# Performance work log

Measured on AMD Instinct MI355X. Metric: run time of the kernel, lower is better.

The kernel has to match this reference:

```python
import jax, jax.numpy as jnp
import numpy as np

GRID_SIZE = 5
SPLINE_ORDER = 3
HIDDEN = 128
IN_FT = 768
BATCH = 32768

def make_grid():
    # uniform grid on [-1, 1] extended by spline_order knots on each side
    h = 2.0 / GRID_SIZE
    return (jnp.arange(-SPLINE_ORDER, GRID_SIZE + SPLINE_ORDER + 1, dtype=jnp.float32) * h - 1.0)

def b_splines(x, grid):
    # x: (B, in) -> bases: (B, in, GRID_SIZE + SPLINE_ORDER) via Cox-de-Boor recursion
    xe = x[..., None]                                  # (B, in, 1)
    bases = ((xe >= grid[:-1]) & (xe < grid[1:])).astype(x.dtype)
    for k in range(1, SPLINE_ORDER + 1):
        left = (xe - grid[:-(k + 1)]) / (grid[k:-1] - grid[:-(k + 1)]) * bases[..., :-1]
        right = (grid[k + 1:] - xe) / (grid[k + 1:] - grid[1:-k]) * bases[..., 1:]
        bases = left + right
    return bases

def kan_layer(x, base_w, spline_w, grid):
    # base_w: (out, in); spline_w: (out, in, G+k)
    B = x.shape[0]
    base_out = jax.nn.silu(x) @ base_w.T
    bas = b_splines(x, grid).reshape(B, -1)            # (B, in*(G+k))
    spline_out = bas @ spline_w.reshape(spline_w.shape[0], -1).T
    return base_out + spline_out

def setup_inputs() -> dict:
    key = jax.random.key(0)
    ks = jax.random.split(key, 8)
    nb = GRID_SIZE + SPLINE_ORDER  # 8 basis functions per edge
    return {
        "stm": jax.random.uniform(ks[0], (BATCH, IN_FT), dtype=jnp.float32),
        "nstm": jax.random.uniform(ks[1], (BATCH, IN_FT), dtype=jnp.float32),
        "ft_w": jax.random.normal(ks[2], (HIDDEN, IN_FT), dtype=jnp.float32) * 0.02,
        "ft_b": jnp.zeros((HIDDEN,), dtype=jnp.float32),
        "kan1_base_w": jax.random.normal(ks[3], (HIDDEN, 2 * HIDDEN), dtype=jnp.float32) * 0.05,
        "kan1_spline_w": jax.random.normal(ks[4], (HIDDEN, 2 * HIDDEN, nb), dtype=jnp.float32) * 0.05,
        "kan2_base_w": jax.random.normal(ks[5], (1, HIDDEN), dtype=jnp.float32) * 0.05,
        "kan2_spline_w": jax.random.normal(ks[6], (1, HIDDEN, nb), dtype=jnp.float32) * 0.05,
    }

def reference(stm, nstm, ft_w, ft_b, kan1_base_w, kan1_spline_w, kan2_base_w, kan2_spline_w):
    grid = make_grid()
    stm_h = stm @ ft_w.T + ft_b
    nstm_h = nstm @ ft_w.T + ft_b
    hidden = jnp.concatenate([stm_h, nstm_h], axis=1)   # (B, 2*HIDDEN)
    hidden = kan_layer(hidden, kan1_base_w, kan1_spline_w, grid)
    out = kan_layer(hidden, kan2_base_w, kan2_spline_w, grid)
    return jax.nn.sigmoid(out)
```

## Files before the change

### kernel.cpp

```cpp
#include <hip/hip_runtime.h>
#include <hip/hip_bf16.h>
#include <math.h>
#include <stdint.h>

typedef __attribute__((ext_vector_type(8))) short bf16x8;
typedef __attribute__((ext_vector_type(4))) float f32x4;

#define SH 260

__device__ __forceinline__ uint32_t pack2(float a, float b) {
    union { __hip_bfloat162 h2; uint32_t u; } c;
    c.h2 = __float22bfloat162_rn(make_float2(a, b));
    return c.u;
}
__device__ __forceinline__ unsigned short f2bf(float f) {
    union { __hip_bfloat16 h; unsigned short u; } c;
    c.h = __float2bfloat16(f);
    return c.u;
}
__device__ __forceinline__ float bf2f(unsigned short h) {
    union { uint32_t u; float f; } c; c.u = ((uint32_t)h) << 16;
    return c.f;
}
__device__ __forceinline__ float silu_f(float x) {
    return x / (1.0f + __expf(-x));
}

__device__ __forceinline__ void bspline8(float x, float* __restrict__ b) {
    const float tt = (x + 2.2f) * 2.5f;
#pragma unroll
    for (int v = 0; v < 8; ++v) {
        float y = fabsf(tt - (float)(v + 2));
        float p = fmaxf(2.0f - y, 0.0f);
        float q = fmaxf(1.0f - y, 0.0f);
        b[v] = (p * p * p - 4.0f * q * q * q) * (1.0f / 6.0f);
    }
}

__device__ __forceinline__ void gload16(const void* g, void* l) {
    __builtin_amdgcn_global_load_lds(
        (const __attribute__((address_space(1))) void*)g,
        (__attribute__((address_space(3))) void*)l, 16, 0, 0);
}

__global__ __launch_bounds__(256) void prep_ftw(const float* __restrict__ ftw,
                                                unsigned short* __restrict__ Wb) {
    const int idx = blockIdx.x * 256 + threadIdx.x;
    Wb[idx] = f2bf(ftw[idx]);
}

__global__ __launch_bounds__(256) void prep_bp(const float* __restrict__ bw,
                                               const float* __restrict__ sw,
                                               unsigned short* __restrict__ Bp) {
    const int idx = blockIdx.x * 256 + threadIdx.x;
    const int n = idx >> 12;
    const int k = idx & 4095;
    const int f = k >> 4;
    const int v = k & 15;
    float val = 0.f;
    if (v == 0) val = bw[n * 256 + f];
    else if (v <= 8) val = sw[(size_t)(n * 256 + f) * 8 + (v - 1)];
    Bp[idx] = f2bf(val);
}

__global__ __launch_bounds__(512) void kan_fused(
        const float* __restrict__ stm, const float* __restrict__ nstm,
        const unsigned short* __restrict__ Wb, const float* __restrict__ bias,
        const unsigned short* __restrict__ Bp,
        const float* __restrict__ w2b, const float* __restrict__ w2s,
        float* __restrict__ out) {
    __shared__ alignas(16) char lds[132096];
    char* smA = lds;
    char* smB = lds + 32768;
    unsigned short* smH = (unsigned short*)(lds + 65536);

    const int r0 = blockIdx.x * 128;
    const int t = threadIdx.x;
    const int l = t & 63, w = t >> 6;
    const int fr = l & 15, h = l >> 4;

    const int wrF = w >> 1, wcF = w & 1;
    const int arowb = w * 16 + (l >> 5);
    const int acol = (l & 31) * 4;

    float4 regY[8];
    f32x4 facc[2][4];
#pragma unroll
    for (int mt = 0; mt < 2; ++mt)
#pragma unroll
        for (int nt = 0; nt < 4; ++nt) facc[mt][nt] = (f32x4){0.f, 0.f, 0.f, 0.f};

#pragma unroll
    for (int q = 0; q < 8; ++q)
        regY[q] = *reinterpret_cast<const float4*>(
            &stm[(size_t)(r0 + arowb + q * 2) * 768 + acol]);

#pragma unroll 1
    for (int tk = 0; tk < 12; ++tk) {
        const int k0 = (tk >= 6 ? tk - 6 : tk) * 128;
#pragma unroll
        for (int q = 0; q < 8; ++q) {
            const int rowA = arowb + q * 2;
            int2 wv;
            wv.x = (int)pack2(regY[q].x, regY[q].y);
            wv.y = (int)pack2(regY[q].z, regY[q].w);
            const uint32_t dst = (uint32_t)rowA * 256u +
                ((uint32_t)((((l & 31) >> 1)) ^ (rowA & 15)) << 4) +
                (uint32_t)(l & 1) * 8u;
            *reinterpret_cast<int2*>(smA + dst) = wv;
        }
#pragma unroll
        for (int j = 0; j < 4; ++j) {
            const int idx = w * 4 + j;
            const int col = idx * 4 + (l >> 4);
            gload16(&Wb[(size_t)col * 768 + k0 + (((l & 15) ^ (col & 15)) << 3)],
                    smB + idx * 1024);
        }
        if (tk < 11) {
            const int nk = tk + 1;
            const float* __restrict__ Ap = (nk >= 6) ? nstm : stm;
            const int nk0 = (nk >= 6 ? nk - 6 : nk) * 128;
#pragma unroll
            for (int q = 0; q < 8; ++q)
                regY[q] = *reinterpret_cast<const float4*>(
                    &Ap[(size_t)(r0 + arowb + q * 2) * 768 + nk0 + acol]);
            asm volatile("s_waitcnt vmcnt(8)" ::: "memory");
        } else {
            asm volatile("s_waitcnt vmcnt(0)" ::: "memory");
        }
        asm volatile("s_waitcnt lgkmcnt(0)" ::: "memory");
        __builtin_amdgcn_sched_barrier(0);
        __builtin_amdgcn_s_barrier();
#pragma unroll
        for (int ks = 0; ks < 4; ++ks) {
            bf16x8 a[2], b[4];
#pragma unroll
            for (int mt = 0; mt < 2; ++mt) {
                const uint32_t row = (uint32_t)(wrF * 32 + mt * 16 + fr);
                a[mt] = *reinterpret_cast<const bf16x8*>(
                    smA + row * 256u +
                    (((uint32_t)(ks * 4 + h) ^ (row & 15u)) << 4));
            }
#pragma unroll
            for (int nt = 0; nt < 4; ++nt) {
                const uint32_t col = (uint32_t)(wcF * 64 + nt * 16 + fr);
                b[nt] = *reinterpret_cast<const bf16x8*>(
                    smB + col * 256u +
                    (((uint32_t)(ks * 4 + h) ^ (col & 15u)) << 4));
            }
#pragma unroll
            for (int mt = 0; mt < 2; ++mt)
#pragma unroll
                for (int nt = 0; nt < 4; ++nt)
                    facc[mt][nt] = __builtin_amdgcn_mfma_f32_16x16x32_bf16(
                        a[mt], b[nt], facc[mt][nt], 0, 0, 0);
        }
        if (tk == 5 || tk == 11) {
            const int so = (tk == 11) ? 128 : 0;
#pragma unroll
            for (int nt = 0; nt < 4; ++nt) {
                const int colL = wcF * 64 + nt * 16 + fr;
                const float bv = bias[colL];
#pragma unroll
                for (int mt = 0; mt < 2; ++mt) {
#pragma unroll
                    for (int j = 0; j < 4; ++j) {
                        const int row = wrF * 32 + mt * 16 + h * 4 + j;
                        smH[row * SH + so + colL] = f2bf(facc[mt][nt][j] + bv);
                    }
                    facc[mt][nt] = (f32x4){0.f, 0.f, 0.f, 0.f};
                }
            }
        }
        asm volatile("s_waitcnt lgkmcnt(0)" ::: "memory");
        __builtin_amdgcn_sched_barrier(0);
        __builtin_amdgcn_s_barrier();
    }

    const int wrK = w >> 2, wcK = w & 3;
    const int xrow = t & 127, xq = t >> 7;
    f32x4 kacc[4][2];
#pragma unroll
    for (int mt = 0; mt < 4; ++mt)
#pragma unroll
        for (int nt = 0; nt < 2; ++nt) kacc[mt][nt] = (f32x4){0.f, 0.f, 0.f, 0.f};

#pragma unroll 1
    for (int jb = 0; jb < 32; ++jb) {
#pragma unroll
        for (int j = 0; j < 4; ++j) {
            const int idx = w * 4 + j;
            const int col = idx * 4 + (l >> 4);
            gload16(&Bp[(size_t)col * 4096 + jb * 128 +
                        (((l & 15) ^ (col & 15)) << 3)],
                    smB + idx * 1024);
        }
        {
            const uint32_t xx = *reinterpret_cast<const uint32_t*>(
                reinterpret_cast<const char*>(smH) +
                ((size_t)xrow * SH + jb * 8 + xq * 2) * 2);
#pragma unroll
            for (int e = 0; e < 2; ++e) {
                const float x =
                    bf2f((unsigned short)(e ? (xx >> 16) : (xx & 0xffffu)));
                float bs[8];
                bspline8(x, bs);
                const uint32_t w0 = pack2(silu_f(x), bs[0]);
                const uint32_t w1 = pack2(bs[1], bs[2]);
                const uint32_t w2 = pack2(bs[3], bs[4]);
                const uint32_t w3 = pack2(bs[5], bs[6]);
                const uint32_t w4 = pack2(bs[7], 0.f);
                const int f = xq * 2 + e;
                const uint32_t base = (uint32_t)xrow * 256u;
                const uint32_t s0 = (uint32_t)((2 * f) ^ (xrow & 15)) << 4;
                const uint32_t s1 = (uint32_t)((2 * f + 1) ^ (xrow & 15)) << 4;
                *reinterpret_cast<int4*>(smA + base + s0) =
                    make_int4((int)w0, (int)w1, (int)w2, (int)w3);
                *reinterpret_cast<int4*>(smA + base + s1) =
                    make_int4((int)w4, 0, 0, 0);
            }
        }
        asm volatile("s_waitcnt vmcnt(0) lgkmcnt(0)" ::: "memory");
        __builtin_amdgcn_sched_barrier(0);
        __builtin_amdgcn_s_barrier();
#pragma unroll
        for (int ks = 0; ks < 4; ++ks) {
            bf16x8 a[4], b[2];
#pragma unroll
            for (int mt = 0; mt < 4; ++mt) {
                const uint32_t row = (uint32_t)(wrK * 64 + mt * 16 + fr);
                a[mt] = *reinterpret_cast<const bf16x8*>(
                    smA + row * 256u +
                    (((uint32_t)(ks * 4 + h) ^ (row & 15u)) << 4));
            }
#pragma unroll
            for (int nt = 0; nt < 2; ++nt) {
                const uint32_t col = (uint32_t)(wcK * 32 + nt * 16 + fr);
                b[nt] = *reinterpret_cast<const bf16x8*>(
                    smB + col * 256u +
                    (((uint32_t)(ks * 4 + h) ^ (col & 15u)) << 4));
            }
#pragma unroll
            for (int mt = 0; mt < 4; ++mt)
#pragma unroll
                for (int nt = 0; nt < 2; ++nt)
                    kacc[mt][nt] = __builtin_amdgcn_mfma_f32_16x16x32_bf16(
                        a[mt], b[nt], kacc[mt][nt], 0, 0, 0);
        }
        asm volatile("s_waitcnt lgkmcnt(0)" ::: "memory");
        __builtin_amdgcn_sched_barrier(0);
        __builtin_amdgcn_s_barrier();
    }

    unsigned short* smH2 = (unsigned short*)lds;
#pragma unroll
    for (int mt = 0; mt < 4; ++mt)
#pragma unroll
        for (int nt = 0; nt < 2; ++nt) {
            const int col = wcK * 32 + nt * 16 + fr;
#pragma unroll
            for (int j = 0; j < 4; ++j) {
                const int row = wrK * 64 + mt * 16 + h * 4 + j;
                smH2[row * 136 + col] = f2bf(kacc[mt][nt][j]);
            }
        }
    __syncthreads();
    const int row2 = t >> 2, qd = t & 3;
    float sum = 0.f;
#pragma unroll 4
    for (int i = 0; i < 32; ++i) {
        const int j = qd * 32 + ((i + qd * 8) & 31);
        const float x = bf2f(smH2[row2 * 136 + j]);
        float bs[8];
        bspline8(x, bs);
        const float4 s0 = *reinterpret_cast<const float4*>(&w2s[j * 8]);
        const float4 s1 = *reinterpret_cast<const float4*>(&w2s[j * 8 + 4]);
        float s = silu_f(x) * w2b[j];
        s += bs[0] * s0.x + bs[1] * s0.y + bs[2] * s0.z + bs[3] * s0.w;
        s += bs[4] * s1.x + bs[5] * s1.y + bs[6] * s1.z + bs[7] * s1.w;
        sum += s;
    }
    sum += __shfl_xor(sum, 1, 64);
    sum += __shfl_xor(sum, 2, 64);
    if (qd == 0) out[r0 + row2] = 1.0f / (1.0f + __expf(-sum));
}

extern "C" void kernel_launch(void* const* d_in, const int* in_sizes, int n_in,
                              void* d_out, int out_size, void* d_ws, size_t ws_size,
                              hipStream_t stream) {
    const float* stm  = (const float*)d_in[0];
    const float* nstm = (const float*)d_in[1];
    const float* ft_w = (const float*)d_in[2];
    const float* ft_b = (const float*)d_in[3];
    const float* k1bw = (const float*)d_in[4];
    const float* k1sw = (const float*)d_in[5];
    const float* k2bw = (const float*)d_in[6];
    const float* k2sw = (const float*)d_in[7];
    float* out = (float*)d_out;

    char* ws = (char*)d_ws;
    unsigned short* Wb = (unsigned short*)ws;
    unsigned short* Bp = (unsigned short*)(ws + 196608);

    prep_ftw<<<384, 256, 0, stream>>>(ft_w, Wb);
    prep_bp<<<2048, 256, 0, stream>>>(k1bw, k1sw, Bp);
    kan_fused<<<256, 512, 0, stream>>>(stm, nstm, Wb, ft_b, Bp, k2bw, k2sw, out);
}
```

Baseline: 115.6 us.

## Halve row tile to 64, double grid, transpose hidden layout, add setprio

The fused kernel now handles 64 rows per block instead of 128 and launches 512 blocks instead of 256. It stores the first-layer hidden activations transposed with a swizzle so each wave expands one feature across 64 rows during the spline stage. LDS use drops from about 129 KB to 80 KB so more blocks can be resident per CU, which should improve latency hiding and balance across the 256 CUs. The feature GEMM loop is unrolled by two with double-buffered register prefetch, and MFMA phases run at raised priority. The trade-off is that each Wb and Bp weight tile is reloaded twice as often, and each MFMA step does less work.

```diff
diff --git a/kernel.cpp b/kernel.cpp
--- a/kernel.cpp
+++ b/kernel.cpp
@@ -5,8 +5,6 @@
 
 typedef __attribute__((ext_vector_type(8))) short bf16x8;
 typedef __attribute__((ext_vector_type(4))) float f32x4;
-
-#define SH 260
 
 __device__ __forceinline__ uint32_t pack2(float a, float b) {
     union { __hip_bfloat162 h2; uint32_t u; } c;
@@ -63,213 +61,212 @@
     Bp[idx] = f2bf(val);
 }
 
-__global__ __launch_bounds__(512) void kan_fused(
+__global__ __launch_bounds__(512, 4) void kan_fused(
         const float* __restrict__ stm, const float* __restrict__ nstm,
         const unsigned short* __restrict__ Wb, const float* __restrict__ bias,
         const unsigned short* __restrict__ Bp,
         const float* __restrict__ w2b, const float* __restrict__ w2s,
         float* __restrict__ out) {
-    __shared__ alignas(16) char lds[132096];
-    char* smA = lds;
-    char* smB = lds + 32768;
-    unsigned short* smH = (unsigned short*)(lds + 65536);
-
-    const int r0 = blockIdx.x * 128;
+    __shared__ alignas(16) char lds[81920];
+    char* smA  = lds;
+    char* smB  = lds + 16384;
+    char* smHT = lds + 49152;
+
+    const int r0 = blockIdx.x * 64;
     const int t = threadIdx.x;
     const int l = t & 63, w = t >> 6;
     const int fr = l & 15, h = l >> 4;
-
-    const int wrF = w >> 1, wcF = w & 1;
-    const int arowb = w * 16 + (l >> 5);
-    const int acol = (l & 31) * 4;
-
-    float4 regY[8];
-    f32x4 facc[2][4];
+    const int wr = w >> 2, wc = w & 3;
+
+    const int arow = t >> 3;
+    const int acol = (t & 7) * 16;
+    const uint32_t adst0 = (uint32_t)arow * 256u +
+        ((uint32_t)(((t & 7) * 2) ^ (arow & 15)) << 4);
+    const uint32_t adst1 = (uint32_t)arow * 256u +
+        ((uint32_t)(((t & 7) * 2 + 1) ^ (arow & 15)) << 4);
+    const int gidx = w * 4;
+
+    f32x4 acc[2][2];
 #pragma unroll
     for (int mt = 0; mt < 2; ++mt)
 #pragma unroll
-        for (int nt = 0; nt < 4; ++nt) facc[mt][nt] = (f32x4){0.f, 0.f, 0.f, 0.f};
-
-#pragma unroll
-    for (int q = 0; q < 8; ++q)
-        regY[q] = *reinterpret_cast<const float4*>(
-            &stm[(size_t)(r0 + arowb + q * 2) * 768 + acol]);
-
+        for (int nt = 0; nt < 2; ++nt) acc[mt][nt] = (f32x4){0.f, 0.f, 0.f, 0.f};
+
+    float4 regY[4], regZ[4];
+
+#define FT_ISSUE(REG, TK)                                                      \
+    {                                                                          \
+        const float* __restrict__ Ap = ((TK) >= 6) ? nstm : stm;               \
+        const int kk = ((TK) % 6) * 128;                                       \
+        _Pragma("unroll") for (int q = 0; q < 4; ++q)                          \
+            REG[q] = *reinterpret_cast<const float4*>(                         \
+                &Ap[(size_t)(r0 + arow) * 768 + kk + acol + q * 4]);           \
+    }
+
+#define FT_WRITE(REG)                                                          \
+    {                                                                          \
+        int4 w0, w1;                                                           \
+        w0.x = (int)pack2(REG[0].x, REG[0].y);                                 \
+        w0.y = (int)pack2(REG[0].z, REG[0].w);                                 \
+        w0.z = (int)pack2(REG[1].x, REG[1].y);                                 \
+        w0.w = (int)pack2(REG[1].z, REG[1].w);                                 \
+        w1.x = (int)pack2(REG[2].x, REG[2].y);                                 \
+        w1.y = (int)pack2(REG[2].z, REG[2].w);                                 \
+        w1.z = (int)pack2(REG[3].x, REG[3].y);                                 \
+        w1.w = (int)pack2(REG[3].z, REG[3].w);                                 \
+        *reinterpret_cast<int4*>(smA + adst0) = w0;                            \
+        *reinterpret_cast<int4*>(smA + adst1) = w1;                            \
+    }
+
+#define GLOADB_FT(K0)                                                          \
+    _Pragma("unroll") for (int j = 0; j < 4; ++j) {                            \
+        const int col = (gidx + j) * 4 + (l >> 4);                             \
+        gload16(&Wb[(size_t)col * 768 + (K0) + (((l & 15) ^ (col & 15)) << 3)],\
+                smB + (gidx + j) * 1024);                                      \
+    }
+
+#define GEMM_STEP()                                                            \
+    _Pragma("unroll") for (int ks = 0; ks < 4; ++ks) {                         \
+        bf16x8 a[2], b[2];                                                     \
+        _Pragma("unroll") for (int mt = 0; mt < 2; ++mt) {                     \
+            const uint32_t row = (uint32_t)(wr * 32 + mt * 16 + fr);           \
+            a[mt] = *reinterpret_cast<const bf16x8*>(                          \
+                smA + row * 256u +                                             \
+                (((uint32_t)(ks * 4 + h) ^ (row & 15u)) << 4));                \
+        }                                                                      \
+        _Pragma("unroll") for (int nt = 0; nt < 2; ++nt) {                     \
+            const uint32_t col = (uint32_t)(wc * 32 + nt * 16 + fr);           \
+            b[nt] = *reinterpret_cast<const bf16x8*>(                          \
+                smB + col * 256u +                                             \
+                (((uint32_t)(ks * 4 + h) ^ (col & 15u)) << 4));                \
+        }                                                                      \
+        _Pragma("unroll") for (int mt = 0; mt < 2; ++mt)                       \
+            _Pragma("unroll") for (int nt = 0; nt < 2; ++nt)                   \
+                acc[mt][nt] = __builtin_amdgcn_mfma_f32_16x16x32_bf16(         \
+                    a[mt], b[nt], acc[mt][nt], 0, 0, 0);                       \
+    }
+
+#define DUMP_H(SO)                                                             \
+    _Pragma("unroll") for (int nt = 0; nt < 2; ++nt) {                         \
+        const int col = wc * 32 + nt * 16 + fr;                                \
+        const float bv = bias[col];                                            \
+        const int feat = (SO) + col;                                           \
+        _Pragma("unroll") for (int mt = 0; mt < 2; ++mt) {                     \
+            const int rowb = wr * 32 + mt * 16 + h * 4;                        \
+            int2 o;                                                            \
+            o.x = (int)pack2(acc[mt][nt][0] + bv, acc[mt][nt][1] + bv);        \
+            o.y = (int)pack2(acc[mt][nt][2] + bv, acc[mt][nt][3] + bv);        \
+            const uint32_t db = (uint32_t)feat * 128u +                        \
+                ((uint32_t)((rowb >> 3) ^ (feat & 7)) << 4) +                  \
+                (uint32_t)(rowb & 7) * 2u;                                     \
+            *reinterpret_cast<int2*>(smHT + db) = o;                           \
+            acc[mt][nt] = (f32x4){0.f, 0.f, 0.f, 0.f};                         \
+        }                                                                      \
+    }
+
+#define LGKM_BAR()                                                             \
+    asm volatile("s_waitcnt lgkmcnt(0)" ::: "memory");                         \
+    __builtin_amdgcn_sched_barrier(0);                                         \
+    __builtin_amdgcn_s_barrier();
+
+    FT_ISSUE(regY, 0);
+    FT_ISSUE(regZ, 1);
 #pragma unroll 1
-    for (int tk = 0; tk < 12; ++tk) {
-        const int k0 = (tk >= 6 ? tk - 6 : tk) * 128;
-#pragma unroll
-        for (int q = 0; q < 8; ++q) {
-            const int rowA = arowb + q * 2;
-            int2 wv;
-            wv.x = (int)pack2(regY[q].x, regY[q].y);
-            wv.y = (int)pack2(regY[q].z, regY[q].w);
-            const uint32_t dst = (uint32_t)rowA * 256u +
-                ((uint32_t)((((l & 31) >> 1)) ^ (rowA & 15)) << 4) +
-                (uint32_t)(l & 1) * 8u;
-            *reinterpret_cast<int2*>(smA + dst) = wv;
-        }
-#pragma unroll
-        for (int j = 0; j < 4; ++j) {
-            const int idx = w * 4 + j;
-            const int col = idx * 4 + (l >> 4);
-            gload16(&Wb[(size_t)col * 768 + k0 + (((l & 15) ^ (col & 15)) << 3)],
-                    smB + idx * 1024);
-        }
-        if (tk < 11) {
-            const int nk = tk + 1;
-            const float* __restrict__ Ap = (nk >= 6) ? nstm : stm;
-            const int nk0 = (nk >= 6 ? nk - 6 : nk) * 128;
-#pragma unroll
-            for (int q = 0; q < 8; ++q)
-                regY[q] = *reinterpret_cast<const float4*>(
-                    &Ap[(size_t)(r0 + arowb + q * 2) * 768 + nk0 + acol]);
-            asm volatile("s_waitcnt vmcnt(8)" ::: "memory");
+    for (int pp = 0; pp < 6; ++pp) {
+        FT_WRITE(regY);
+        GLOADB_FT(((2 * pp) % 6) * 128);
+        __builtin_amdgcn_sched_barrier(0);
+        if (pp < 5) {
+            FT_ISSUE(regY, 2 * pp + 2);
+            asm volatile("s_waitcnt vmcnt(4)" ::: "memory");
         } else {
             asm volatile("s_waitcnt vmcnt(0)" ::: "memory");
         }
         asm volatile("s_waitcnt lgkmcnt(0)" ::: "memory");
         __builtin_amdgcn_sched_barrier(0);
         __builtin_amdgcn_s_barrier();
-#pragma unroll
-        for (int ks = 0; ks < 4; ++ks) {
-            bf16x8 a[2], b[4];
-#pragma unroll
-            for (int mt = 0; mt < 2; ++mt) {
-                const uint32_t row = (uint32_t)(wrF * 32 + mt * 16 + fr);
-                a[mt] = *reinterpret_cast<const bf16x8*>(
-                    smA + row * 256u +
-                    (((uint32_t)(ks * 4 + h) ^ (row & 15u)) << 4));
-            }
-#pragma unroll
-            for (int nt = 0; nt < 4; ++nt) {
-                const uint32_t col = (uint32_t)(wcF * 64 + nt * 16 + fr);
-                b[nt] = *reinterpret_cast<const bf16x8*>(
-                    smB + col * 256u +
-                    (((uint32_t)(ks * 4 + h) ^ (col & 15u)) << 4));
-            }
-#pragma unroll
-            for (int mt = 0; mt < 2; ++mt)
-#pragma unroll
-                for (int nt = 0; nt < 4; ++nt)
-                    facc[mt][nt] = __builtin_amdgcn_mfma_f32_16x16x32_bf16(
-                        a[mt], b[nt], facc[mt][nt], 0, 0, 0);
-        }
-        if (tk == 5 || tk == 11) {
-            const int so = (tk == 11) ? 128 : 0;
-#pragma unroll
-            for (int nt = 0; nt < 4; ++nt) {
-                const int colL = wcF * 64 + nt * 16 + fr;
-                const float bv = bias[colL];
-#pragma unroll
-                for (int mt = 0; mt < 2; ++mt) {
-#pragma unroll
-                    for (int j = 0; j < 4; ++j) {
-                        const int row = wrF * 32 + mt * 16 + h * 4 + j;
-                        smH[row * SH + so + colL] = f2bf(facc[mt][nt][j] + bv);
-                    }
-                    facc[mt][nt] = (f32x4){0.f, 0.f, 0.f, 0.f};
-                }
-            }
+        __builtin_amdgcn_s_setprio(1);
+        GEMM_STEP();
+        __builtin_amdgcn_s_setprio(0);
+        LGKM_BAR();
+        FT_WRITE(regZ);
+        GLOADB_FT(((2 * pp + 1) % 6) * 128);
+        __builtin_amdgcn_sched_barrier(0);
+        if (pp < 5) {
+            FT_ISSUE(regZ, 2 * pp + 3);
+            asm volatile("s_waitcnt vmcnt(4)" ::: "memory");
+        } else {
+            asm volatile("s_waitcnt vmcnt(0)" ::: "memory");
         }
         asm volatile("s_waitcnt lgkmcnt(0)" ::: "memory");
         __builtin_amdgcn_sched_barrier(0);
         __builtin_amdgcn_s_barrier();
-    }
-
-    const int wrK = w >> 2, wcK = w & 3;
-    const int xrow = t & 127, xq = t >> 7;
-    f32x4 kacc[4][2];
-#pragma unroll
-    for (int mt = 0; mt < 4; ++mt)
-#pragma unroll
-        for (int nt = 0; nt < 2; ++nt) kacc[mt][nt] = (f32x4){0.f, 0.f, 0.f, 0.f};
+        __builtin_amdgcn_s_setprio(1);
+        GEMM_STEP();
+        __builtin_amdgcn_s_setprio(0);
+        if (pp == 2) { DUMP_H(0); }
+        if (pp == 5) { DUMP_H(128); }
+        LGKM_BAR();
+    }
 
 #pragma unroll 1
     for (int jb = 0; jb < 32; ++jb) {
 #pragma unroll
         for (int j = 0; j < 4; ++j) {
-            const int idx = w * 4 + j;
-            const int col = idx * 4 + (l >> 4);
+            const int col = (gidx + j) * 4 + (l >> 4);
             gload16(&Bp[(size_t)col * 4096 + jb * 128 +
                         (((l & 15) ^ (col & 15)) << 3)],
-                    smB + idx * 1024);
-        }
+                    smB + (gidx + j) * 1024);
+        }
+        __builtin_amdgcn_sched_barrier(0);
         {
-            const uint32_t xx = *reinterpret_cast<const uint32_t*>(
-                reinterpret_cast<const char*>(smH) +
-                ((size_t)xrow * SH + jb * 8 + xq * 2) * 2);
-#pragma unroll
-            for (int e = 0; e < 2; ++e) {
-                const float x =
-                    bf2f((unsigned short)(e ? (xx >> 16) : (xx & 0xffffu)));
-                float bs[8];
-                bspline8(x, bs);
-                const uint32_t w0 = pack2(silu_f(x), bs[0]);
-                const uint32_t w1 = pack2(bs[1], bs[2]);
-                const uint32_t w2 = pack2(bs[3], bs[4]);
-                const uint32_t w3 = pack2(bs[5], bs[6]);
-                const uint32_t w4 = pack2(bs[7], 0.f);
-                const int f = xq * 2 + e;
-                const uint32_t base = (uint32_t)xrow * 256u;
-                const uint32_t s0 = (uint32_t)((2 * f) ^ (xrow & 15)) << 4;
-                const uint32_t s1 = (uint32_t)((2 * f + 1) ^ (xrow & 15)) << 4;
-                *reinterpret_cast<int4*>(smA + base + s0) =
-                    make_int4((int)w0, (int)w1, (int)w2, (int)w3);
-                *reinterpret_cast<int4*>(smA + base + s1) =
-                    make_int4((int)w4, 0, 0, 0);
+            const int feat = jb * 8 + w;
+            const unsigned short xv = *reinterpret_cast<const unsigned short*>(
+                smHT + (uint32_t)feat * 128u +
+                ((uint32_t)((l >> 3) ^ (feat & 7)) << 4) + (uint32_t)(l & 7) * 2u);
+            const float x = bf2f(xv);
+            float bs[8];
+            bspline8(x, bs);
+            const uint32_t pw0 = pack2(silu_f(x), bs[0]);
+            const uint32_t pw1 = pack2(bs[1], bs[2]);
+            const uint32_t pw2 = pack2(bs[3], bs[4]);
+            const uint32_t pw3 = pack2(bs[5], bs[6]);
+            const uint32_t pw4 = pack2(bs[7], 0.f);
+            const uint32_t d0 = (uint32_t)l * 256u +
+                ((uint32_t)((2 * w) ^ (l & 15)) << 4);
+            const uint32_t d1 = (uint32_t)l * 256u +
+                ((uint32_t)((2 * w + 1) ^ (l & 15)) << 4);
+            *reinterpret_cast<int4*>(smA + d0) =
+                make_int4((int)pw0, (int)pw1, (int)pw2, (int)pw3);
+            *reinterpret_cast<int4*>(smA + d1) = make_int4((int)pw4, 0, 0, 0);
+        }
+        asm volatile("s_waitcnt vmcnt(0) lgkmcnt(0)" ::: "memory");
+        __builtin_amdgcn_sched_barrier(0);
+        __builtin_amdgcn_s_barrier();
+        __builtin_amdgcn_s_setprio(1);
+        GEMM_STEP();
+        __builtin_amdgcn_s_setprio(0);
+        LGKM_BAR();
+    }
+
+    unsigned short* smH2 = (unsigned short*)lds;
+#pragma unroll
+    for (int mt = 0; mt < 2; ++mt)
+#pragma unroll
+        for (int nt = 0; nt < 2; ++nt) {
+            const int col = wc * 32 + nt * 16 + fr;
+#pragma unroll
+            for (int j = 0; j < 4; ++j) {
+                const int row = wr * 32 + mt * 16 + h * 4 + j;
+                smH2[row * 136 + col] = f2bf(acc[mt][nt][j]);
             }
         }
-        asm volatile("s_waitcnt vmcnt(0) lgkmcnt(0)" ::: "memory");
-        __builtin_amdgcn_sched_barrier(0);
-        __builtin_amdgcn_s_barrier();
-#pragma unroll
-        for (int ks = 0; ks < 4; ++ks) {
-            bf16x8 a[4], b[2];
-#pragma unroll
-            for (int mt = 0; mt < 4; ++mt) {
-                const uint32_t row = (uint32_t)(wrK * 64 + mt * 16 + fr);
-                a[mt] = *reinterpret_cast<const bf16x8*>(
-                    smA + row * 256u +
-                    (((uint32_t)(ks * 4 + h) ^ (row & 15u)) << 4));
-            }
-#pragma unroll
-            for (int nt = 0; nt < 2; ++nt) {
-                const uint32_t col = (uint32_t)(wcK * 32 + nt * 16 + fr);
-                b[nt] = *reinterpret_cast<const bf16x8*>(
-                    smB + col * 256u +
-                    (((uint32_t)(ks * 4 + h) ^ (col & 15u)) << 4));
-            }
-#pragma unroll
-            for (int mt = 0; mt < 4; ++mt)
-#pragma unroll
-                for (int nt = 0; nt < 2; ++nt)
-                    kacc[mt][nt] = __builtin_amdgcn_mfma_f32_16x16x32_bf16(
-                        a[mt], b[nt], kacc[mt][nt], 0, 0, 0);
-        }
-        asm volatile("s_waitcnt lgkmcnt(0)" ::: "memory");
-        __builtin_amdgcn_sched_barrier(0);
-        __builtin_amdgcn_s_barrier();
-    }
-
-    unsigned short* smH2 = (unsigned short*)lds;
-#pragma unroll
-    for (int mt = 0; mt < 4; ++mt)
-#pragma unroll
-        for (int nt = 0; nt < 2; ++nt) {
-            const int col = wcK * 32 + nt * 16 + fr;
-#pragma unroll
-            for (int j = 0; j < 4; ++j) {
-                const int row = wrK * 64 + mt * 16 + h * 4 + j;
-                smH2[row * 136 + col] = f2bf(kacc[mt][nt][j]);
-            }
-        }
     __syncthreads();
-    const int row2 = t >> 2, qd = t & 3;
+    const int row2 = t >> 3, qd = t & 7;
     float sum = 0.f;
 #pragma unroll 4
-    for (int i = 0; i < 32; ++i) {
-        const int j = qd * 32 + ((i + qd * 8) & 31);
+    for (int i = 0; i < 16; ++i) {
+        const int j = qd * 16 + ((i + qd * 2) & 15);
         const float x = bf2f(smH2[row2 * 136 + j]);
         float bs[8];
         bspline8(x, bs);
@@ -282,6 +279,7 @@
     }
     sum += __shfl_xor(sum, 1, 64);
     sum += __shfl_xor(sum, 2, 64);
+    sum += __shfl_xor(sum, 4, 64);
     if (qd == 0) out[r0 + row2] = 1.0f / (1.0f + __expf(-sum));
 }
 
@@ -304,5 +302,5 @@
 
     prep_ftw<<<384, 256, 0, stream>>>(ft_w, Wb);
     prep_bp<<<2048, 256, 0, stream>>>(k1bw, k1sw, Bp);
-    kan_fused<<<256, 512, 0, stream>>>(stm, nstm, Wb, ft_b, Bp, k2bw, k2sw, out);
-}
+    kan_fused<<<512, 512, 0, stream>>>(stm, nstm, Wb, ft_b, Bp, k2bw, k2sw, out);
+}
```

Result: faster. 105.6 us (median of 2 runs) (-8.7%).

## Split feature GEMM by stm/nstm halves and restructure KAN1 MFMA tiling

Applied to the files above, without the earlier changes.

The feature-transformer GEMM now processes stm and nstm concurrently: waves 0-3 handle stm and 4-7 handle nstm with 64-wide K steps and larger 4x4 MFMA tiles per wave. Results go into a transposed swizzled hidden buffer. The KAN1 GEMM now uses only four waves with 4x4 tiles while all eight waves compute the basis expansion. It also adds setprio around MFMA bursts and asks launch_bounds for two blocks per CU. The goal is better register reuse per MFMA and fewer K iterations, at the cost of idle waves during the second GEMM and higher register pressure.

```diff
diff --git a/kernel.cpp b/kernel.cpp
--- a/kernel.cpp
+++ b/kernel.cpp
@@ -5,8 +5,6 @@
 
 typedef __attribute__((ext_vector_type(8))) short bf16x8;
 typedef __attribute__((ext_vector_type(4))) float f32x4;
-
-#define SH 260
 
 __device__ __forceinline__ uint32_t pack2(float a, float b) {
     union { __hip_bfloat162 h2; uint32_t u; } c;
@@ -63,67 +61,92 @@
     Bp[idx] = f2bf(val);
 }
 
-__global__ __launch_bounds__(512) void kan_fused(
+__global__ __launch_bounds__(512, 2) void kan_fused(
         const float* __restrict__ stm, const float* __restrict__ nstm,
         const unsigned short* __restrict__ Wb, const float* __restrict__ bias,
         const unsigned short* __restrict__ Bp,
         const float* __restrict__ w2b, const float* __restrict__ w2s,
         float* __restrict__ out) {
-    __shared__ alignas(16) char lds[132096];
-    char* smA = lds;
-    char* smB = lds + 32768;
-    unsigned short* smH = (unsigned short*)(lds + 65536);
+    __shared__ alignas(16) char lds[131072];
+    char* smA0 = lds;
+    char* smA1 = lds + 16384;
+    char* smB  = lds + 32768;
+    char* smB2 = lds + 32768;
+    char* phi  = lds;
+    char* smHT = lds + 65536;
 
     const int r0 = blockIdx.x * 128;
     const int t = threadIdx.x;
     const int l = t & 63, w = t >> 6;
     const int fr = l & 15, h = l >> 4;
 
-    const int wrF = w >> 1, wcF = w & 1;
-    const int arowb = w * 16 + (l >> 5);
-    const int acol = (l & 31) * 4;
+    const int s1 = w >> 2;
+    const int wrF = (w >> 1) & 1;
+    const int wcF = w & 1;
+
+    const int arow = t >> 2;
+    const int aq = t & 3;
+    const uint32_t aw0 = (uint32_t)arow * 128u +
+        ((uint32_t)((aq * 2) ^ (arow & 7)) << 4);
+    const uint32_t aw1 = (uint32_t)arow * 128u +
+        ((uint32_t)((aq * 2 + 1) ^ (arow & 7)) << 4);
+
+    f32x4 acc[4][4];
+#pragma unroll
+    for (int mt = 0; mt < 4; ++mt)
+#pragma unroll
+        for (int nt = 0; nt < 4; ++nt) acc[mt][nt] = (f32x4){0.f, 0.f, 0.f, 0.f};
 
     float4 regY[8];
-    f32x4 facc[2][4];
-#pragma unroll
-    for (int mt = 0; mt < 2; ++mt)
-#pragma unroll
-        for (int nt = 0; nt < 4; ++nt) facc[mt][nt] = (f32x4){0.f, 0.f, 0.f, 0.f};
-
-#pragma unroll
-    for (int q = 0; q < 8; ++q)
-        regY[q] = *reinterpret_cast<const float4*>(
-            &stm[(size_t)(r0 + arowb + q * 2) * 768 + acol]);
-
+
+#define FT_ISSUE(TK)                                                           \
+    {                                                                          \
+        const size_t gb = (size_t)(r0 + arow) * 768 + (TK) * 64 + aq * 16;     \
+        _Pragma("unroll") for (int q = 0; q < 4; ++q)                          \
+            regY[q] = *reinterpret_cast<const float4*>(&stm[gb + q * 4]);      \
+        _Pragma("unroll") for (int q = 0; q < 4; ++q)                          \
+            regY[4 + q] = *reinterpret_cast<const float4*>(&nstm[gb + q * 4]); \
+    }
+
+#define FT_WRITE()                                                             \
+    {                                                                          \
+        int4 u0, u1;                                                           \
+        u0.x = (int)pack2(regY[0].x, regY[0].y);                               \
+        u0.y = (int)pack2(regY[0].z, regY[0].w);                               \
+        u0.z = (int)pack2(regY[1].x, regY[1].y);                               \
+        u0.w = (int)pack2(regY[1].z, regY[1].w);                               \
+        u1.x = (int)pack2(regY[2].x, regY[2].y);                               \
+        u1.y = (int)pack2(regY[2].z, regY[2].w);                               \
+        u1.z = (int)pack2(regY[3].x, regY[3].y);                               \
+        u1.w = (int)pack2(regY[3].z, regY[3].w);                               \
+        *reinterpret_cast<int4*>(smA0 + aw0) = u0;                             \
+        *reinterpret_cast<int4*>(smA0 + aw1) = u1;                             \
+        u0.x = (int)pack2(regY[4].x, regY[4].y);                               \
+        u0.y = (int)pack2(regY[4].z, regY[4].w);                               \
+        u0.z = (int)pack2(regY[5].x, regY[5].y);                               \
+        u0.w = (int)pack2(regY[5].z, regY[5].w);                               \
+        u1.x = (int)pack2(regY[6].x, regY[6].y);                               \
+        u1.y = (int)pack2(regY[6].z, regY[6].w);                               \
+        u1.z = (int)pack2(regY[7].x, regY[7].y);                               \
+        u1.w = (int)pack2(regY[7].z, regY[7].w);                               \
+        *reinterpret_cast<int4*>(smA1 + aw0) = u0;                             \
+        *reinterpret_cast<int4*>(smA1 + aw1) = u1;                             \
+    }
+
+    FT_ISSUE(0);
 #pragma unroll 1
     for (int tk = 0; tk < 12; ++tk) {
-        const int k0 = (tk >= 6 ? tk - 6 : tk) * 128;
-#pragma unroll
-        for (int q = 0; q < 8; ++q) {
-            const int rowA = arowb + q * 2;
-            int2 wv;
-            wv.x = (int)pack2(regY[q].x, regY[q].y);
-            wv.y = (int)pack2(regY[q].z, regY[q].w);
-            const uint32_t dst = (uint32_t)rowA * 256u +
-                ((uint32_t)((((l & 31) >> 1)) ^ (rowA & 15)) << 4) +
-                (uint32_t)(l & 1) * 8u;
-            *reinterpret_cast<int2*>(smA + dst) = wv;
-        }
-#pragma unroll
-        for (int j = 0; j < 4; ++j) {
-            const int idx = w * 4 + j;
-            const int col = idx * 4 + (l >> 4);
-            gload16(&Wb[(size_t)col * 768 + k0 + (((l & 15) ^ (col & 15)) << 3)],
-                    smB + idx * 1024);
-        }
+        FT_WRITE();
+#pragma unroll
+        for (int j = 0; j < 2; ++j) {
+            const int i = w * 2 + j;
+            const int col = i * 8 + (l >> 3);
+            gload16(&Wb[(size_t)col * 768 + tk * 64 + (((l & 7) ^ (col & 7)) << 3)],
+                    smB + i * 1024);
+        }
+        __builtin_amdgcn_sched_barrier(0);
         if (tk < 11) {
-            const int nk = tk + 1;
-            const float* __restrict__ Ap = (nk >= 6) ? nstm : stm;
-            const int nk0 = (nk >= 6 ? nk - 6 : nk) * 128;
-#pragma unroll
-            for (int q = 0; q < 8; ++q)
-                regY[q] = *reinterpret_cast<const float4*>(
-                    &Ap[(size_t)(r0 + arowb + q * 2) * 768 + nk0 + acol]);
+            FT_ISSUE(tk + 1);
             asm volatile("s_waitcnt vmcnt(8)" ::: "memory");
         } else {
             asm volatile("s_waitcnt vmcnt(0)" ::: "memory");
@@ -131,139 +154,147 @@
         asm volatile("s_waitcnt lgkmcnt(0)" ::: "memory");
         __builtin_amdgcn_sched_barrier(0);
         __builtin_amdgcn_s_barrier();
-#pragma unroll
-        for (int ks = 0; ks < 4; ++ks) {
-            bf16x8 a[2], b[4];
-#pragma unroll
-            for (int mt = 0; mt < 2; ++mt) {
-                const uint32_t row = (uint32_t)(wrF * 32 + mt * 16 + fr);
+        const char* As = s1 ? smA1 : smA0;
+        __builtin_amdgcn_s_setprio(1);
+#pragma unroll
+        for (int ks = 0; ks < 2; ++ks) {
+            bf16x8 a[4], b[4];
+#pragma unroll
+            for (int mt = 0; mt < 4; ++mt) {
+                const uint32_t row = (uint32_t)(wrF * 64 + mt * 16 + fr);
                 a[mt] = *reinterpret_cast<const bf16x8*>(
-                    smA + row * 256u +
-                    (((uint32_t)(ks * 4 + h) ^ (row & 15u)) << 4));
+                    As + row * 128u + (((uint32_t)(ks * 4 + h) ^ (row & 7u)) << 4));
             }
 #pragma unroll
             for (int nt = 0; nt < 4; ++nt) {
                 const uint32_t col = (uint32_t)(wcF * 64 + nt * 16 + fr);
                 b[nt] = *reinterpret_cast<const bf16x8*>(
-                    smB + col * 256u +
-                    (((uint32_t)(ks * 4 + h) ^ (col & 15u)) << 4));
+                    smB + col * 128u + (((uint32_t)(ks * 4 + h) ^ (col & 7u)) << 4));
             }
 #pragma unroll
-            for (int mt = 0; mt < 2; ++mt)
+            for (int mt = 0; mt < 4; ++mt)
 #pragma unroll
                 for (int nt = 0; nt < 4; ++nt)
-                    facc[mt][nt] = __builtin_amdgcn_mfma_f32_16x16x32_bf16(
-                        a[mt], b[nt], facc[mt][nt], 0, 0, 0);
-        }
-        if (tk == 5 || tk == 11) {
-            const int so = (tk == 11) ? 128 : 0;
+                    acc[mt][nt] = __builtin_amdgcn_mfma_f32_16x16x32_bf16(
+                        a[mt], b[nt], acc[mt][nt], 0, 0, 0);
+        }
+        __builtin_amdgcn_s_setprio(0);
+        asm volatile("s_waitcnt lgkmcnt(0)" ::: "memory");
+        __builtin_amdgcn_sched_barrier(0);
+        __builtin_amdgcn_s_barrier();
+    }
+#pragma unroll
+    for (int nt = 0; nt < 4; ++nt) {
+        const int col = wcF * 64 + nt * 16 + fr;
+        const float bv = bias[col];
+        const int feat = s1 * 128 + col;
+#pragma unroll
+        for (int mt = 0; mt < 4; ++mt) {
+            const int rowb = wrF * 64 + mt * 16 + h * 4;
+            int2 o;
+            o.x = (int)pack2(acc[mt][nt][0] + bv, acc[mt][nt][1] + bv);
+            o.y = (int)pack2(acc[mt][nt][2] + bv, acc[mt][nt][3] + bv);
+            const uint32_t db = (uint32_t)feat * 256u +
+                ((uint32_t)((rowb >> 3) ^ (feat & 15)) << 4) +
+                (uint32_t)(rowb & 7) * 2u;
+            *reinterpret_cast<int2*>(smHT + db) = o;
+            acc[mt][nt] = (f32x4){0.f, 0.f, 0.f, 0.f};
+        }
+    }
+    asm volatile("s_waitcnt lgkmcnt(0)" ::: "memory");
+    __builtin_amdgcn_sched_barrier(0);
+    __builtin_amdgcn_s_barrier();
+
+    const int erow = t & 127;
+    const int ef = t >> 7;
+    const int wr2 = (w >> 1) & 1;
+    const int wc2 = w & 1;
+
+#pragma unroll 1
+    for (int jb = 0; jb < 32; ++jb) {
+#pragma unroll
+        for (int j = 0; j < 4; ++j) {
+            const int i = w * 4 + j;
+            const int col = i * 4 + (l >> 4);
+            gload16(&Bp[(size_t)col * 4096 + jb * 128 +
+                        (((l & 15) ^ (col & 15)) << 3)],
+                    smB2 + i * 1024);
+        }
+        __builtin_amdgcn_sched_barrier(0);
+#pragma unroll
+        for (int e = 0; e < 2; ++e) {
+            const int f = ef + e * 4;
+            const int feat = jb * 8 + f;
+            const unsigned short xv = *reinterpret_cast<const unsigned short*>(
+                smHT + (uint32_t)feat * 256u +
+                ((uint32_t)((erow >> 3) ^ (feat & 15)) << 4) +
+                (uint32_t)(erow & 7) * 2u);
+            const float x = bf2f(xv);
+            float bs[8];
+            bspline8(x, bs);
+            const uint32_t p0 = pack2(silu_f(x), bs[0]);
+            const uint32_t p1 = pack2(bs[1], bs[2]);
+            const uint32_t p2 = pack2(bs[3], bs[4]);
+            const uint32_t p3 = pack2(bs[5], bs[6]);
+            const uint32_t p4 = pack2(bs[7], 0.f);
+            const uint32_t d0 = (uint32_t)erow * 256u +
+                ((uint32_t)((2 * f) ^ (erow & 15)) << 4);
+            const uint32_t d1 = (uint32_t)erow * 256u +
+                ((uint32_t)((2 * f + 1) ^ (erow & 15)) << 4);
+            *reinterpret_cast<int4*>(phi + d0) =
+                make_int4((int)p0, (int)p1, (int)p2, (int)p3);
+            *reinterpret_cast<int4*>(phi + d1) = make_int4((int)p4, 0, 0, 0);
+        }
+        asm volatile("s_waitcnt vmcnt(0) lgkmcnt(0)" ::: "memory");
+        __builtin_amdgcn_sched_barrier(0);
+        __builtin_amdgcn_s_barrier();
+        if (w < 4) {
+            __builtin_amdgcn_s_setprio(1);
+#pragma unroll
+            for (int ks = 0; ks < 4; ++ks) {
+                bf16x8 a[4], b[4];
+#pragma unroll
+                for (int mt = 0; mt < 4; ++mt) {
+                    const uint32_t row = (uint32_t)(wr2 * 64 + mt * 16 + fr);
+                    a[mt] = *reinterpret_cast<const bf16x8*>(
+                        phi + row * 256u +
+                        (((uint32_t)(ks * 4 + h) ^ (row & 15u)) << 4));
+                }
+#pragma unroll
+                for (int nt = 0; nt < 4; ++nt) {
+                    const uint32_t col = (uint32_t)(wc2 * 64 + nt * 16 + fr);
+                    b[nt] = *reinterpret_cast<const bf16x8*>(
+                        smB2 + col * 256u +
+                        (((uint32_t)(ks * 4 + h) ^ (col & 15u)) << 4));
+                }
+#pragma unroll
+                for (int mt = 0; mt < 4; ++mt)
+#pragma unroll
+                    for (int nt = 0; nt < 4; ++nt)
+                        acc[mt][nt] = __builtin_amdgcn_mfma_f32_16x16x32_bf16(
+                            a[mt], b[nt], acc[mt][nt], 0, 0, 0);
+            }
+            __builtin_amdgcn_s_setprio(0);
+        }
+        asm volatile("s_waitcnt lgkmcnt(0)" ::: "memory");
+        __builtin_amdgcn_sched_barrier(0);
+        __builtin_amdgcn_s_barrier();
+    }
+
+    unsigned short* smH2 = (unsigned short*)lds;
+    if (w < 4) {
+#pragma unroll
+        for (int mt = 0; mt < 4; ++mt)
 #pragma unroll
             for (int nt = 0; nt < 4; ++nt) {
-                const int colL = wcF * 64 + nt * 16 + fr;
-                const float bv = bias[colL];
-#pragma unroll
-                for (int mt = 0; mt < 2; ++mt) {
-#pragma unroll
-                    for (int j = 0; j < 4; ++j) {
-                        const int row = wrF * 32 + mt * 16 + h * 4 + j;
-                        smH[row * SH + so + colL] = f2bf(facc[mt][nt][j] + bv);
-                    }
-                    facc[mt][nt] = (f32x4){0.f, 0.f, 0.f, 0.f};
+                const int col = wc2 * 64 + nt * 16 + fr;
+#pragma unroll
+                for (int j = 0; j < 4; ++j) {
+                    const int row = wr2 * 64 + mt * 16 + h * 4 + j;
+                    smH2[row * 136 + col] = f2bf(acc[mt][nt][j]);
                 }
             }
-        }
-        asm volatile("s_waitcnt lgkmcnt(0)" ::: "memory");
-        __builtin_amdgcn_sched_barrier(0);
-        __builtin_amdgcn_s_barrier();
-    }
-
-    const int wrK = w >> 2, wcK = w & 3;
-    const int xrow = t & 127, xq = t >> 7;
-    f32x4 kacc[4][2];
-#pragma unroll
-    for (int mt = 0; mt < 4; ++mt)
-#pragma unroll
-        for (int nt = 0; nt < 2; ++nt) kacc[mt][nt] = (f32x4){0.f, 0.f, 0.f, 0.f};
-
-#pragma unroll 1
-    for (int jb = 0; jb < 32; ++jb) {
-#pragma unroll
-        for (int j = 0; j < 4; ++j) {
-            const int idx = w * 4 + j;
-            const int col = idx * 4 + (l >> 4);
-            gload16(&Bp[(size_t)col * 4096 + jb * 128 +
-                        (((l & 15) ^ (col & 15)) << 3)],
-                    smB + idx * 1024);
-        }
-        {
-            const uint32_t xx = *reinterpret_cast<const uint32_t*>(
-                reinterpret_cast<const char*>(smH) +
-                ((size_t)xrow * SH + jb * 8 + xq * 2) * 2);
-#pragma unroll
-            for (int e = 0; e < 2; ++e) {
-                const float x =
-                    bf2f((unsigned short)(e ? (xx >> 16) : (xx & 0xffffu)));
-                float bs[8];
-                bspline8(x, bs);
-                const uint32_t w0 = pack2(silu_f(x), bs[0]);
-                const uint32_t w1 = pack2(bs[1], bs[2]);
-                const uint32_t w2 = pack2(bs[3], bs[4]);
-                const uint32_t w3 = pack2(bs[5], bs[6]);
-                const uint32_t w4 = pack2(bs[7], 0.f);
-                const int f = xq * 2 + e;
-                const uint32_t base = (uint32_t)xrow * 256u;
-                const uint32_t s0 = (uint32_t)((2 * f) ^ (xrow & 15)) << 4;
-                const uint32_t s1 = (uint32_t)((2 * f + 1) ^ (xrow & 15)) << 4;
-                *reinterpret_cast<int4*>(smA + base + s0) =
-                    make_int4((int)w0, (int)w1, (int)w2, (int)w3);
-                *reinterpret_cast<int4*>(smA + base + s1) =
-                    make_int4((int)w4, 0, 0, 0);
-            }
-        }
-        asm volatile("s_waitcnt vmcnt(0) lgkmcnt(0)" ::: "memory");
-        __builtin_amdgcn_sched_barrier(0);
-        __builtin_amdgcn_s_barrier();
-#pragma unroll
-        for (int ks = 0; ks < 4; ++ks) {
-            bf16x8 a[4], b[2];
-#pragma unroll
-            for (int mt = 0; mt < 4; ++mt) {
-                const uint32_t row = (uint32_t)(wrK * 64 + mt * 16 + fr);
-                a[mt] = *reinterpret_cast<const bf16x8*>(
-                    smA + row * 256u +
-                    (((uint32_t)(ks * 4 + h) ^ (row & 15u)) << 4));
-            }
-#pragma unroll
-            for (int nt = 0; nt < 2; ++nt) {
-                const uint32_t col = (uint32_t)(wcK * 32 + nt * 16 + fr);
-                b[nt] = *reinterpret_cast<const bf16x8*>(
-                    smB + col * 256u +
-                    (((uint32_t)(ks * 4 + h) ^ (col & 15u)) << 4));
-            }
-#pragma unroll
-            for (int mt = 0; mt < 4; ++mt)
-#pragma unroll
-                for (int nt = 0; nt < 2; ++nt)
-                    kacc[mt][nt] = __builtin_amdgcn_mfma_f32_16x16x32_bf16(
-                        a[mt], b[nt], kacc[mt][nt], 0, 0, 0);
-        }
-        asm volatile("s_waitcnt lgkmcnt(0)" ::: "memory");
-        __builtin_amdgcn_sched_barrier(0);
-        __builtin_amdgcn_s_barrier();
-    }
-
-    unsigned short* smH2 = (unsigned short*)lds;
-#pragma unroll
-    for (int mt = 0; mt < 4; ++mt)
-#pragma unroll
-        for (int nt = 0; nt < 2; ++nt) {
-            const int col = wcK * 32 + nt * 16 + fr;
-#pragma unroll
-            for (int j = 0; j < 4; ++j) {
-                const int row = wrK * 64 + mt * 16 + h * 4 + j;
-                smH2[row * 136 + col] = f2bf(kacc[mt][nt][j]);
-            }
-        }
+    }
     __syncthreads();
     const int row2 = t >> 2, qd = t & 3;
     float sum = 0.f;
```

New measurement: 115.8 us. No clear change (+0.2%).
